# Kernel optimization log

Hardware: AMD Instinct MI355X
Metric: run time of the kernel (lower is better)

Reference implementation:

```python
import jax, jax.numpy as jnp
import numpy as np

N, C_IN, C_OUT = 8192, 256, 128
TEMP = 1.0
EDGE_P = 0.01  # Bernoulli edge probability -> avg degree ~82


def setup_inputs() -> dict:
    key = jax.random.key(0)
    k_x, k_adj, k_w, k_v0, k_v1 = jax.random.split(key, 5)
    node_feats = jax.random.normal(k_x, (N, C_IN), dtype=jnp.float32)
    adj_matrix = (jax.random.uniform(k_adj, (N, N)) < EDGE_P).astype(jnp.float32)
    lim_w = np.sqrt(6.0 / (C_IN + C_OUT))
    W = jax.random.uniform(k_w, (C_IN, C_OUT), minval=-lim_w, maxval=lim_w, dtype=jnp.float32)
    b = jnp.zeros((C_OUT,), dtype=jnp.float32)
    lim_v = np.sqrt(6.0 / (C_OUT + 1))
    v0 = jax.random.uniform(k_v0, (C_OUT,), minval=-lim_v, maxval=lim_v, dtype=jnp.float32)
    v1 = jax.random.uniform(k_v1, (C_OUT,), minval=-lim_v, maxval=lim_v, dtype=jnp.float32)
    return {"node_feats": node_feats, "adj_matrix": adj_matrix, "W": W, "b": b, "v0": v0, "v1": v1}


def reference(node_feats, adj_matrix, W, b, v0, v1):
    # h: [N, c_out]
    h = node_feats @ W + b
    f1 = h @ v0  # [N]
    f2 = h @ v1  # [N]
    # attn_logits = adj * (f1_i + f2_j); adj==0 entries become exact zeros,
    # which torch's .to_sparse() drops -> sparse softmax normalizes only
    # over edges (adj != 0), and empty rows densify to all-zero rows.
    logits = adj_matrix * (f1[:, None] + f2[None, :])
    vals = (jax.nn.sigmoid(logits) - 0.5) / TEMP
    mask = adj_matrix != 0
    masked = jnp.where(mask, vals, -jnp.inf)
    row_max = jnp.max(masked, axis=1, keepdims=True)
    row_max = jnp.where(jnp.isfinite(row_max), row_max, 0.0)  # guard empty rows
    e = jnp.where(mask, jnp.exp(masked - row_max), 0.0)
    denom = jnp.sum(e, axis=1, keepdims=True)
    attn_probs = e / jnp.maximum(denom, jnp.finfo(e.dtype).tiny)  # empty rows -> 0
    return attn_probs @ h
```

## Files before the change

kernel.cpp:

```cpp
#include <hip/hip_runtime.h>
#include <math.h>

#define NN    8192
#define CIN   256
#define COUT  128
#define MAXEG 256
#define P1BLK 2048

typedef unsigned uvec4 __attribute__((ext_vector_type(4)));

__global__ __launch_bounds__(256) void k1_gemm(
    const float* __restrict__ X, const float* __restrict__ W,
    const float* __restrict__ b, const float* __restrict__ v0,
    const float* __restrict__ v1,
    float* __restrict__ h, float* __restrict__ f1, float* __restrict__ f2)
{
    __shared__ float Xs[16][32];
    const int tid = threadIdx.x;
    const int ct  = tid & 63;
    const int rg  = tid >> 6;
    const int c   = ct * 2;
    const int row0 = blockIdx.x * 16;

    float acc[4][2] = {{0.f,0.f},{0.f,0.f},{0.f,0.f},{0.f,0.f}};

    for (int kc = 0; kc < CIN; kc += 32) {
        if (tid < 128) {
            const int r = tid >> 3, q = tid & 7;
            const float4 xv = *(const float4*)(X + (size_t)(row0 + r) * CIN + kc + q * 4);
            *(float4*)&Xs[r][q * 4] = xv;
        }
        float2 wv[32];
        #pragma unroll
        for (int kk = 0; kk < 32; ++kk)
            wv[kk] = *(const float2*)(W + (size_t)(kc + kk) * COUT + c);
        __syncthreads();

        #pragma unroll
        for (int rr = 0; rr < 4; ++rr) {
            const int lr = rg * 4 + rr;
            #pragma unroll
            for (int k4 = 0; k4 < 8; ++k4) {
                const float4 xv = *(const float4*)&Xs[lr][k4 * 4];
                acc[rr][0] += xv.x * wv[k4*4+0].x; acc[rr][1] += xv.x * wv[k4*4+0].y;
                acc[rr][0] += xv.y * wv[k4*4+1].x; acc[rr][1] += xv.y * wv[k4*4+1].y;
                acc[rr][0] += xv.z * wv[k4*4+2].x; acc[rr][1] += xv.z * wv[k4*4+2].y;
                acc[rr][0] += xv.w * wv[k4*4+3].x; acc[rr][1] += xv.w * wv[k4*4+3].y;
            }
        }
        __syncthreads();
    }

    const float b0 = b[c], b1 = b[c+1];
    const float v00 = v0[c], v01 = v0[c+1];
    const float v10 = v1[c], v11 = v1[c+1];

    #pragma unroll
    for (int rr = 0; rr < 4; ++rr) {
        const int row = row0 + rg * 4 + rr;
        const float h0 = acc[rr][0] + b0;
        const float h1 = acc[rr][1] + b1;
        *(float2*)(h + (size_t)row * COUT + c) = make_float2(h0, h1);
        float p0 = h0 * v00 + h1 * v01;
        float p1 = h0 * v10 + h1 * v11;
        #pragma unroll
        for (int off = 32; off; off >>= 1) {
            p0 += __shfl_down(p0, off, 64);
            p1 += __shfl_down(p1, off, 64);
        }
        if (ct == 0) { f1[row] = p0; f2[row] = p1; }
    }
}

__global__ __launch_bounds__(256) void k_bitmap(
    const uvec4* __restrict__ adj4, unsigned char* __restrict__ bm)
{
    const unsigned gtid = blockIdx.x * 256 + threadIdx.x;
    #pragma unroll 4
    for (int it = 0; it < 16; ++it) {
        const size_t base = (size_t)it * (P1BLK * 256) + gtid;
        const uvec4 a = adj4[base * 2];
        const uvec4 b = adj4[base * 2 + 1];
        const unsigned m =
            (a.x ? 1u   : 0u) | (a.y ? 2u   : 0u) | (a.z ? 4u   : 0u) | (a.w ? 8u   : 0u) |
            (b.x ? 16u  : 0u) | (b.y ? 32u  : 0u) | (b.z ? 64u  : 0u) | (b.w ? 128u : 0u);
        bm[base] = (unsigned char)m;
    }
}

__global__ __launch_bounds__(256) void k2_attn(
    const unsigned* __restrict__ bm, const float* __restrict__ h,
    const float* __restrict__ f1, const float* __restrict__ f2,
    float* __restrict__ out)
{
    __shared__ unsigned short sjl[4][MAXEG];
    __shared__ float vl[4][MAXEG];

    const int tid  = threadIdx.x;
    const int wid  = tid >> 6;
    const int lane = tid & 63;
    const int row  = blockIdx.x * 4 + wid;
    const int c    = lane * 2;

    const uvec4 w4 = ((const uvec4*)(bm + (size_t)row * 256))[lane];
    unsigned wa[4] = { w4.x, w4.y, w4.z, w4.w };

    const int lc = __popc(wa[0]) + __popc(wa[1]) + __popc(wa[2]) + __popc(wa[3]);
    int pre = lc;
    #pragma unroll
    for (int off = 1; off < 64; off <<= 1) {
        const int t = __shfl_up(pre, off, 64);
        if (lane >= off) pre += t;
    }
    unsigned p = (unsigned)(pre - lc);
    const int n0 = __shfl(pre, 63, 64);
    const int n  = min(n0, MAXEG);

    const int jb = lane * 128;
    #pragma unroll
    for (int k = 0; k < 4; ++k) {
        unsigned mm = wa[k];
        while (mm) {
            const int bit = __builtin_ctz(mm);
            mm &= mm - 1;
            if (p < MAXEG) sjl[wid][p] = (unsigned short)(jb + k * 32 + bit);
            ++p;
        }
    }

    if (n == 0) {
        *(float2*)(out + (size_t)row * COUT + c) = make_float2(0.f, 0.f);
        return;
    }
    asm volatile("s_waitcnt lgkmcnt(0)" ::: "memory");

    const float f1i = f1[row];
    float m = -1e30f;
    #pragma unroll
    for (int q = 0; q < 4; ++q) {
        const int pp = lane + q * 64;
        if (pp < n) {
            const float x = f1i + f2[sjl[wid][pp]];
            const float s = 1.f / (1.f + __expf(-x)) - 0.5f;
            vl[wid][pp] = s;
            m = fmaxf(m, s);
        }
    }
    #pragma unroll
    for (int off = 32; off; off >>= 1) m = fmaxf(m, __shfl_xor(m, off, 64));

    float ssum = 0.f;
    #pragma unroll
    for (int q = 0; q < 4; ++q) {
        const int pp = lane + q * 64;
        if (pp < n) {
            const float e = __expf(vl[wid][pp] - m);
            vl[wid][pp] = e;
            ssum += e;
        }
    }
    #pragma unroll
    for (int off = 32; off; off >>= 1) ssum += __shfl_xor(ssum, off, 64);
    const float inv = 1.f / ssum;
    asm volatile("s_waitcnt lgkmcnt(0)" ::: "memory");

    float ax = 0.f, ay = 0.f;
    int q = 0;
    for (; q + 7 < n; q += 8) {
        int   jj[8];
        float ww[8];
        float2 aa[8];
        #pragma unroll
        for (int u = 0; u < 8; ++u) { jj[u] = sjl[wid][q + u]; ww[u] = vl[wid][q + u]; }
        #pragma unroll
        for (int u = 0; u < 8; ++u) aa[u] = *(const float2*)(h + (size_t)jj[u] * COUT + c);
        #pragma unroll
        for (int u = 0; u < 8; ++u) { ax += ww[u] * aa[u].x; ay += ww[u] * aa[u].y; }
    }
    for (; q < n; ++q) {
        const int   j = sjl[wid][q];
        const float w = vl[wid][q];
        const float2 a = *(const float2*)(h + (size_t)j * COUT + c);
        ax += w * a.x;
        ay += w * a.y;
    }
    *(float2*)(out + (size_t)row * COUT + c) = make_float2(ax * inv, ay * inv);
}

extern "C" void kernel_launch(void* const* d_in, const int* in_sizes, int n_in,
                              void* d_out, int out_size, void* d_ws, size_t ws_size,
                              hipStream_t stream) {
    const float* X   = (const float*)d_in[0];
    const float* adj = (const float*)d_in[1];
    const float* W   = (const float*)d_in[2];
    const float* b   = (const float*)d_in[3];
    const float* v0  = (const float*)d_in[4];
    const float* v1  = (const float*)d_in[5];
    float* out = (float*)d_out;

    float*         h  = (float*)d_ws;
    float*         f1 = h + (size_t)NN * COUT;
    float*         f2 = f1 + NN;
    unsigned char* bm = (unsigned char*)(f2 + NN);

    k1_gemm<<<NN / 16, 256, 0, stream>>>(X, W, b, v0, v1, h, f1, f2);
    k_bitmap<<<P1BLK, 256, 0, stream>>>((const uvec4*)adj, bm);
    k2_attn<<<NN / 4, 256, 0, stream>>>((const unsigned*)bm, h, f1, f2, out);
}
```

Baseline: 98.00 us.

## Merge GEMM and adjacency bitmap kernels into one launch with nontemporal loads

Result: slower. 100.4 us (+2.4%).

```diff
diff --git a/kernel.cpp b/kernel.cpp
--- a/kernel.cpp
+++ b/kernel.cpp
@@ -5,86 +5,92 @@
 #define CIN   256
 #define COUT  128
 #define MAXEG 256
-#define P1BLK 2048
+#define NK1   512
+#define NBM   512
 
 typedef unsigned uvec4 __attribute__((ext_vector_type(4)));
 
-__global__ __launch_bounds__(256) void k1_gemm(
-    const float* __restrict__ X, const float* __restrict__ W,
-    const float* __restrict__ b, const float* __restrict__ v0,
-    const float* __restrict__ v1,
-    float* __restrict__ h, float* __restrict__ f1, float* __restrict__ f2)
+__global__ __launch_bounds__(256) void kAB(
+    const float* __restrict__ X, const float* __restrict__ adj,
+    const float* __restrict__ W, const float* __restrict__ b,
+    const float* __restrict__ v0, const float* __restrict__ v1,
+    float* __restrict__ h, float* __restrict__ f1, float* __restrict__ f2,
+    unsigned char* __restrict__ bm)
 {
-    __shared__ float Xs[16][32];
     const int tid = threadIdx.x;
-    const int ct  = tid & 63;
-    const int rg  = tid >> 6;
-    const int c   = ct * 2;
-    const int row0 = blockIdx.x * 16;
-
-    float acc[4][2] = {{0.f,0.f},{0.f,0.f},{0.f,0.f},{0.f,0.f}};
-
-    for (int kc = 0; kc < CIN; kc += 32) {
-        if (tid < 128) {
-            const int r = tid >> 3, q = tid & 7;
-            const float4 xv = *(const float4*)(X + (size_t)(row0 + r) * CIN + kc + q * 4);
-            *(float4*)&Xs[r][q * 4] = xv;
-        }
-        float2 wv[32];
-        #pragma unroll
-        for (int kk = 0; kk < 32; ++kk)
-            wv[kk] = *(const float2*)(W + (size_t)(kc + kk) * COUT + c);
-        __syncthreads();
+
+    if (blockIdx.x < NK1) {
+        __shared__ float Xs[16][32];
+        const int ct  = tid & 63;
+        const int rg  = tid >> 6;
+        const int c   = ct * 2;
+        const int row0 = blockIdx.x * 16;
+
+        float acc[4][2] = {{0.f,0.f},{0.f,0.f},{0.f,0.f},{0.f,0.f}};
+
+        for (int kc = 0; kc < CIN; kc += 32) {
+            if (tid < 128) {
+                const int r = tid >> 3, q = tid & 7;
+                const float4 xv = *(const float4*)(X + (size_t)(row0 + r) * CIN + kc + q * 4);
+                *(float4*)&Xs[r][q * 4] = xv;
+            }
+            float2 wv[32];
+            #pragma unroll
+            for (int kk = 0; kk < 32; ++kk)
+                wv[kk] = *(const float2*)(W + (size_t)(kc + kk) * COUT + c);
+            __syncthreads();
+
+            #pragma unroll
+            for (int rr = 0; rr < 4; ++rr) {
+                const int lr = rg * 4 + rr;
+                #pragma unroll
+                for (int k4 = 0; k4 < 8; ++k4) {
+                    const float4 xv = *(const float4*)&Xs[lr][k4 * 4];
+                    acc[rr][0] += xv.x * wv[k4*4+0].x; acc[rr][1] += xv.x * wv[k4*4+0].y;
+                    acc[rr][0] += xv.y * wv[k4*4+1].x; acc[rr][1] += xv.y * wv[k4*4+1].y;
+                    acc[rr][0] += xv.z * wv[k4*4+2].x; acc[rr][1] += xv.z * wv[k4*4+2].y;
+                    acc[rr][0] += xv.w * wv[k4*4+3].x; acc[rr][1] += xv.w * wv[k4*4+3].y;
+                }
+            }
+            __syncthreads();
+        }
+
+        const float b0 = b[c], b1 = b[c+1];
+        const float v00 = v0[c], v01 = v0[c+1];
+        const float v10 = v1[c], v11 = v1[c+1];
 
         #pragma unroll
         for (int rr = 0; rr < 4; ++rr) {
-            const int lr = rg * 4 + rr;
+            const int row = row0 + rg * 4 + rr;
+            const float h0 = acc[rr][0] + b0;
+            const float h1 = acc[rr][1] + b1;
+            *(float2*)(h + (size_t)row * COUT + c) = make_float2(h0, h1);
+            float p0 = h0 * v00 + h1 * v01;
+            float p1 = h0 * v10 + h1 * v11;
             #pragma unroll
-            for (int k4 = 0; k4 < 8; ++k4) {
-                const float4 xv = *(const float4*)&Xs[lr][k4 * 4];
-                acc[rr][0] += xv.x * wv[k4*4+0].x; acc[rr][1] += xv.x * wv[k4*4+0].y;
-                acc[rr][0] += xv.y * wv[k4*4+1].x; acc[rr][1] += xv.y * wv[k4*4+1].y;
-                acc[rr][0] += xv.z * wv[k4*4+2].x; acc[rr][1] += xv.z * wv[k4*4+2].y;
-                acc[rr][0] += xv.w * wv[k4*4+3].x; acc[rr][1] += xv.w * wv[k4*4+3].y;
+            for (int off = 32; off; off >>= 1) {
+                p0 += __shfl_down(p0, off, 64);
+                p1 += __shfl_down(p1, off, 64);
             }
-        }
-        __syncthreads();
-    }
-
-    const float b0 = b[c], b1 = b[c+1];
-    const float v00 = v0[c], v01 = v0[c+1];
-    const float v10 = v1[c], v11 = v1[c+1];
-
-    #pragma unroll
-    for (int rr = 0; rr < 4; ++rr) {
-        const int row = row0 + rg * 4 + rr;
-        const float h0 = acc[rr][0] + b0;
-        const float h1 = acc[rr][1] + b1;
-        *(float2*)(h + (size_t)row * COUT + c) = make_float2(h0, h1);
-        float p0 = h0 * v00 + h1 * v01;
-        float p1 = h0 * v10 + h1 * v11;
-        #pragma unroll
-        for (int off = 32; off; off >>= 1) {
-            p0 += __shfl_down(p0, off, 64);
-            p1 += __shfl_down(p1, off, 64);
-        }
-        if (ct == 0) { f1[row] = p0; f2[row] = p1; }
-    }
-}
-
-__global__ __launch_bounds__(256) void k_bitmap(
-    const uvec4* __restrict__ adj4, unsigned char* __restrict__ bm)
-{
-    const unsigned gtid = blockIdx.x * 256 + threadIdx.x;
-    #pragma unroll 4
-    for (int it = 0; it < 16; ++it) {
-        const size_t base = (size_t)it * (P1BLK * 256) + gtid;
-        const uvec4 a = adj4[base * 2];
-        const uvec4 b = adj4[base * 2 + 1];
-        const unsigned m =
-            (a.x ? 1u   : 0u) | (a.y ? 2u   : 0u) | (a.z ? 4u   : 0u) | (a.w ? 8u   : 0u) |
-            (b.x ? 16u  : 0u) | (b.y ? 32u  : 0u) | (b.z ? 64u  : 0u) | (b.w ? 128u : 0u);
-        bm[base] = (unsigned char)m;
+            if (ct == 0) { f1[row] = p0; f2[row] = p1; }
+        }
+    } else {
+        const int bb   = blockIdx.x - NK1;
+        const int wid  = tid >> 6;
+        const int lane = tid & 63;
+        const int ws   = bb * 4 + wid;
+        const uvec4* wp = (const uvec4*)adj + (size_t)ws * 8192 + lane * 2;
+        unsigned char* bp = bm + (size_t)ws * 4096 + lane;
+
+        #pragma unroll 8
+        for (int i = 0; i < 64; ++i) {
+            const uvec4 a = __builtin_nontemporal_load(wp + i * 128);
+            const uvec4 d = __builtin_nontemporal_load(wp + i * 128 + 1);
+            const unsigned m =
+                (a.x ? 1u  : 0u) | (a.y ? 2u  : 0u) | (a.z ? 4u  : 0u) | (a.w ? 8u   : 0u) |
+                (d.x ? 16u : 0u) | (d.y ? 32u : 0u) | (d.z ? 64u : 0u) | (d.w ? 128u : 0u);
+            bp[i * 64] = (unsigned char)m;
+        }
     }
 }
 
@@ -203,7 +209,6 @@
     float*         f2 = f1 + NN;
     unsigned char* bm = (unsigned char*)(f2 + NN);
 
-    k1_gemm<<<NN / 16, 256, 0, stream>>>(X, W, b, v0, v1, h, f1, f2);
-    k_bitmap<<<P1BLK, 256, 0, stream>>>((const uvec4*)adj, bm);
+    kAB<<<NK1 + NBM, 256, 0, stream>>>(X, adj, W, b, v0, v1, h, f1, f2, bm);
     k2_attn<<<NN / 4, 256, 0, stream>>>((const unsigned*)bm, h, f1, f2, out);
 }
```
